# Performance work log

Hardware: AMD Instinct MI355X
Metric: run time of the kernel (lower is better)

Reference implementation:

```python
import jax, jax.numpy as jnp
import numpy as np

D = 1024
H = 16
HD = D // H
INNER = 4 * D
EPS = 1e-5


def layernorm(x, g, b):
    mu = jnp.mean(x, axis=-1, keepdims=True)
    var = jnp.mean(jnp.square(x - mu), axis=-1, keepdims=True)
    return (x - mu) * jax.lax.rsqrt(var + EPS) * g + b


def setup_inputs() -> dict:
    key = jax.random.key(0)
    ks = jax.random.split(key, 12)
    s = 0.02
    return {
        "x": jax.random.normal(ks[0], (2, 2048, D), dtype=jnp.float32),
        "ln1_g": jnp.ones((D,), jnp.float32),
        "ln1_b": jnp.zeros((D,), jnp.float32),
        "Wq": jax.random.normal(ks[1], (D, D), jnp.float32) * s,
        "Wk": jax.random.normal(ks[2], (D, D), jnp.float32) * s,
        "Wv": jax.random.normal(ks[3], (D, D), jnp.float32) * s,
        "Wo": jax.random.normal(ks[4], (D, D), jnp.float32) * s,
        "ln2_g": jnp.ones((D,), jnp.float32),
        "ln2_b": jnp.zeros((D,), jnp.float32),
        "W_up": jax.random.normal(ks[5], (D, INNER), jnp.float32) * s,
        "b_up": jnp.zeros((INNER,), jnp.float32),
        "W_down": jax.random.normal(ks[6], (INNER, D), jnp.float32) * s,
        "b_down": jnp.zeros((D,), jnp.float32),
    }


def reference(x, ln1_g, ln1_b, Wq, Wk, Wv, Wo, ln2_g, ln2_b, W_up, b_up, W_down, b_down):
    B, T, C = x.shape
    # --- attention sub-block (pre-norm) ---
    h = layernorm(x, ln1_g, ln1_b)
    q = (h @ Wq).reshape(B, T, H, HD).transpose(0, 2, 1, 3)  # [B,H,T,HD]
    k = (h @ Wk).reshape(B, T, H, HD).transpose(0, 2, 1, 3)
    v = (h @ Wv).reshape(B, T, H, HD).transpose(0, 2, 1, 3)
    scores = jnp.einsum("bhqd,bhkd->bhqk", q, k) / jnp.sqrt(jnp.float32(HD))
    causal = jnp.tril(jnp.ones((T, T), dtype=bool))
    scores = jnp.where(causal, scores, jnp.finfo(scores.dtype).min)
    weights = jax.nn.softmax(scores, axis=-1)
    ctx = jnp.einsum("bhqk,bhkd->bhqd", weights, v)
    y = ctx.transpose(0, 2, 1, 3).reshape(B, T, C) @ Wo
    x = x + y
    # --- MLP sub-block (pre-norm) ---
    h2 = layernorm(x, ln2_g, ln2_b)
    m = jax.nn.gelu(h2 @ W_up + b_up, approximate=False)  # nn.GELU() default = exact erf
    x = x + (m @ W_down + b_down)
    return x
```

## Files before the change

### kernel.cpp

```cpp
#include <hip/hip_runtime.h>
#include <hip/hip_bf16.h>
#include <math.h>

constexpr int Dm = 1024;
constexpr int Tt = 2048;
constexpr int NB = 2;
constexpr int NHd = 16;
constexpr int HDd = 64;
constexpr int FF = 4096;
constexpr int NTOK = NB * Tt;

typedef __attribute__((ext_vector_type(8))) short bf16x8;
typedef __attribute__((ext_vector_type(4))) float f32x4;

struct alignas(8) bh4 { __hip_bfloat16 x, y, z, w; };

#define GLOAD16(gp, lp)                                                        \
  __builtin_amdgcn_global_load_lds(                                            \
      (const __attribute__((address_space(1))) void*)(gp),                     \
      (__attribute__((address_space(3))) void*)(lp), 16, 0, 0)

__device__ __forceinline__ float wave_sum(float v) {
#pragma unroll
  for (int off = 32; off > 0; off >>= 1) v += __shfl_xor(v, off, 64);
  return v;
}

__device__ __forceinline__ float gelu_f(float x) {
  return 0.5f * x * (1.0f + erff(x * 0.7071067811865475f));
}

__global__ __launch_bounds__(256) void ln_kernel(
    const float* __restrict__ x, const float* __restrict__ g,
    const float* __restrict__ b, __hip_bfloat16* __restrict__ out) {
  __shared__ float red[8];
  const int row = blockIdx.x;
  const int t = threadIdx.x;
  const float4 v = reinterpret_cast<const float4*>(x + (size_t)row * Dm)[t];
  float s = v.x + v.y + v.z + v.w;
  s = wave_sum(s);
  if ((t & 63) == 0) red[t >> 6] = s;
  __syncthreads();
  const float mu = (red[0] + red[1] + red[2] + red[3]) * (1.0f / Dm);
  const float dx = v.x - mu, dy = v.y - mu, dz = v.z - mu, dw = v.w - mu;
  float sq = dx * dx + dy * dy + dz * dz + dw * dw;
  sq = wave_sum(sq);
  if ((t & 63) == 0) red[4 + (t >> 6)] = sq;
  __syncthreads();
  const float var = (red[4] + red[5] + red[6] + red[7]) * (1.0f / Dm);
  const float rstd = 1.0f / sqrtf(var + 1e-5f);
  const float4 gv = reinterpret_cast<const float4*>(g)[t];
  const float4 bv = reinterpret_cast<const float4*>(b)[t];
  bh4 o;
  o.x = __float2bfloat16(dx * rstd * gv.x + bv.x);
  o.y = __float2bfloat16(dy * rstd * gv.y + bv.y);
  o.z = __float2bfloat16(dz * rstd * gv.z + bv.z);
  o.w = __float2bfloat16(dw * rstd * gv.w + bv.w);
  *(bh4*)&out[(size_t)row * Dm + t * 4] = o;
}

__global__ __launch_bounds__(256) void wt_kernel(
    const float* __restrict__ W, __hip_bfloat16* __restrict__ Wt,
    int K, int N) {
  __shared__ float tile[32][33];
  const int n0 = blockIdx.x * 32, k0 = blockIdx.y * 32;
  const int tx = threadIdx.x & 31, ty = threadIdx.x >> 5;
#pragma unroll
  for (int r = 0; r < 4; ++r)
    tile[ty + 8 * r][tx] = W[(size_t)(k0 + ty + 8 * r) * N + n0 + tx];
  __syncthreads();
#pragma unroll
  for (int r = 0; r < 4; ++r)
    Wt[(size_t)(n0 + ty + 8 * r) * K + k0 + tx] =
        __float2bfloat16(tile[tx][ty + 8 * r]);
}

enum { EP_QKV = 0, EP_RESID = 1, EP_GELU = 2, EP_DOWN = 3 };

template <int EP>
__global__ __launch_bounds__(256) void gemm_bf16(
    const __hip_bfloat16* __restrict__ A, const __hip_bfloat16* __restrict__ Bt,
    void* __restrict__ Cout, int N, int K,
    const float* __restrict__ bias, const float* __restrict__ resid) {
  __shared__ alignas(16) __hip_bfloat16 As[128 * 64];
  __shared__ alignas(16) __hip_bfloat16 Bs[128 * 64];
  const int t = threadIdx.x;
  const int wave = t >> 6, lane = t & 63;
  const int m0 = blockIdx.x * 128, n0 = blockIdx.y * 128;
  const int wm = wave >> 1, wn = wave & 1;
  const int srow = wave * 32 + (lane >> 3);
  const int scol = (lane & 7) * 8;
  const __hip_bfloat16* Ag = A + (size_t)(m0 + srow) * K + scol;
  const __hip_bfloat16* Bg = Bt + (size_t)(n0 + srow) * K + scol;
  const int lr = lane & 15, lk = lane >> 4;
  f32x4 acc[4][4] = {};
  for (int k0 = 0; k0 < K; k0 += 64) {
#pragma unroll
    for (int i = 0; i < 4; ++i) {
      GLOAD16(Ag + (size_t)i * 8 * K + k0, &As[wave * 2048 + i * 512]);
      GLOAD16(Bg + (size_t)i * 8 * K + k0, &Bs[wave * 2048 + i * 512]);
    }
    __syncthreads();
#pragma unroll
    for (int ks = 0; ks < 2; ++ks) {
      bf16x8 af[4], bf[4];
#pragma unroll
      for (int mi = 0; mi < 4; ++mi)
        af[mi] = *(const bf16x8*)&As[(wm * 64 + mi * 16 + lr) * 64 + ks * 32 + lk * 8];
#pragma unroll
      for (int ni = 0; ni < 4; ++ni)
        bf[ni] = *(const bf16x8*)&Bs[(wn * 64 + ni * 16 + lr) * 64 + ks * 32 + lk * 8];
#pragma unroll
      for (int mi = 0; mi < 4; ++mi)
#pragma unroll
        for (int ni = 0; ni < 4; ++ni)
          acc[mi][ni] = __builtin_amdgcn_mfma_f32_16x16x32_bf16(
              af[mi], bf[ni], acc[mi][ni], 0, 0, 0);
    }
    __syncthreads();
  }
#pragma unroll
  for (int mi = 0; mi < 4; ++mi) {
#pragma unroll
    for (int ni = 0; ni < 4; ++ni) {
      const int col = n0 + wn * 64 + ni * 16 + lr;
      const int row0 = m0 + wm * 64 + mi * 16 + lk * 4;
#pragma unroll
      for (int j = 0; j < 4; ++j) {
        const int row = row0 + j;
        const float v = acc[mi][ni][j];
        if (EP == EP_QKV) {
          const int which = col >> 10, cc = col & 1023;
          const int head = cc >> 6, hd = cc & 63;
          const int bb = row >> 11, tt2 = row & 2047;
          ((__hip_bfloat16*)Cout)[(size_t)which * (4u << 20) +
              ((size_t)(bb * NHd + head) * Tt + tt2) * HDd + hd] =
              __float2bfloat16(v);
        } else if (EP == EP_RESID) {
          ((float*)Cout)[(size_t)row * N + col] =
              v + resid[(size_t)row * N + col];
        } else if (EP == EP_GELU) {
          ((__hip_bfloat16*)Cout)[(size_t)row * N + col] =
              __float2bfloat16(gelu_f(v + bias[col]));
        } else {
          ((float*)Cout)[(size_t)row * N + col] =
              v + bias[col] + resid[(size_t)row * N + col];
        }
      }
    }
  }
}

__global__ __launch_bounds__(256) void attn_mfma(
    const __hip_bfloat16* __restrict__ Q, const __hip_bfloat16* __restrict__ K,
    const __hip_bfloat16* __restrict__ V, __hip_bfloat16* __restrict__ ctx) {
  __shared__ alignas(16) __hip_bfloat16 Ks[64 * 64];
  __shared__ alignas(16) __hip_bfloat16 VTs[64 * 72];
  __shared__ alignas(16) __hip_bfloat16 Pl[4 * 16 * 72];
  const int qt = (int)gridDim.x - 1 - (int)blockIdx.x;
  const int bh = blockIdx.y;
  const int t = threadIdx.x;
  const int w = t >> 6, l = t & 63;
  const int r = l & 15, g = l >> 4;
  const size_t base = (size_t)bh * (size_t)Tt * HDd;
  bf16x8 qf[2];
  {
    const __hip_bfloat16* qrow = Q + base + (size_t)(qt * 64 + w * 16 + r) * HDd;
    qf[0] = *(const bf16x8*)(qrow + g * 8);
    qf[1] = *(const bf16x8*)(qrow + 32 + g * 8);
  }
  float mrun[4], lrun[4];
  f32x4 oacc[4];
#pragma unroll
  for (int j = 0; j < 4; ++j) { mrun[j] = -1e30f; lrun[j] = 0.0f; }
#pragma unroll
  for (int db = 0; db < 4; ++db) oacc[db] = f32x4{0.f, 0.f, 0.f, 0.f};

  for (int kt = 0; kt <= qt; ++kt) {
    __syncthreads();
    {
      const int kr = t >> 3;
      const int cb = (t & 7) ^ (kr & 7);
#pragma unroll
      for (int i = 0; i < 2; ++i)
        GLOAD16(K + base + (size_t)(kt * 64 + i * 32 + kr) * HDd + cb * 8,
                (char*)Ks + i * 4096 + t * 16);
    }
    {
      const int kv = t >> 2, d0 = (t & 3) * 16;
      const __hip_bfloat16* vr = V + base + (size_t)(kt * 64 + kv) * HDd + d0;
      const bf16x8 v0 = *(const bf16x8*)vr;
      const bf16x8 v1 = *(const bf16x8*)(vr + 8);
      short* vts = (short*)VTs;
#pragma unroll
      for (int j = 0; j < 8; ++j) {
        vts[(d0 + j) * 72 + (kv ^ (j << 3))] = v0[j];
        vts[(d0 + 8 + j) * 72 + (kv ^ (j << 3))] = v1[j];
      }
    }
    __syncthreads();
    f32x4 sacc[4];
#pragma unroll
    for (int c4 = 0; c4 < 4; ++c4) sacc[c4] = f32x4{0.f, 0.f, 0.f, 0.f};
#pragma unroll
    for (int c4 = 0; c4 < 4; ++c4) {
      const int krow = c4 * 16 + r;
#pragma unroll
      for (int ks = 0; ks < 2; ++ks) {
        const int cb = (ks * 4 + g) ^ (krow & 7);
        const bf16x8 kf = *(const bf16x8*)&Ks[krow * 64 + cb * 8];
        sacc[c4] = __builtin_amdgcn_mfma_f32_16x16x32_bf16(
            qf[ks], kf, sacc[c4], 0, 0, 0);
      }
    }
    float sc[4][4];
#pragma unroll
    for (int c4 = 0; c4 < 4; ++c4)
#pragma unroll
      for (int j = 0; j < 4; ++j) {
        float s = sacc[c4][j] * 0.125f;
        if (kt == qt && (c4 * 16 + r) > (w * 16 + g * 4 + j)) s = -1e30f;
        sc[c4][j] = s;
      }
#pragma unroll
    for (int j = 0; j < 4; ++j) {
      float mj = fmaxf(fmaxf(sc[0][j], sc[1][j]), fmaxf(sc[2][j], sc[3][j]));
      mj = fmaxf(mj, __shfl_xor(mj, 1, 64));
      mj = fmaxf(mj, __shfl_xor(mj, 2, 64));
      mj = fmaxf(mj, __shfl_xor(mj, 4, 64));
      mj = fmaxf(mj, __shfl_xor(mj, 8, 64));
      const float mn = fmaxf(mrun[j], mj);
      const float corr = __expf(mrun[j] - mn);
      float rs = 0.0f;
#pragma unroll
      for (int c4 = 0; c4 < 4; ++c4) {
        const float p = __expf(sc[c4][j] - mn);
        rs += p;
        Pl[w * 1152 + (g * 4 + j) * 72 + c4 * 16 + r] = __float2bfloat16(p);
      }
      rs += __shfl_xor(rs, 1, 64);
      rs += __shfl_xor(rs, 2, 64);
      rs += __shfl_xor(rs, 4, 64);
      rs += __shfl_xor(rs, 8, 64);
      lrun[j] = lrun[j] * corr + rs;
      mrun[j] = mn;
#pragma unroll
      for (int db = 0; db < 4; ++db) oacc[db][j] *= corr;
    }
#pragma unroll
    for (int kh = 0; kh < 2; ++kh) {
      const bf16x8 pa = *(const bf16x8*)&Pl[w * 1152 + r * 72 + kh * 32 + g * 8];
#pragma unroll
      for (int db = 0; db < 4; ++db) {
        const int d = db * 16 + r;
        const int cb = (kh * 4 + g) ^ (d & 7);
        const bf16x8 vf = *(const bf16x8*)&VTs[d * 72 + cb * 8];
        oacc[db] = __builtin_amdgcn_mfma_f32_16x16x32_bf16(
            pa, vf, oacc[db], 0, 0, 0);
      }
    }
  }
  const int b = bh >> 4, hh = bh & 15;
#pragma unroll
  for (int j = 0; j < 4; ++j) {
    const float inv = 1.0f / lrun[j];
    const size_t tok = (size_t)b * Tt + qt * 64 + w * 16 + g * 4 + j;
#pragma unroll
    for (int db = 0; db < 4; ++db)
      ctx[tok * Dm + hh * 64 + db * 16 + r] =
          __float2bfloat16(oacc[db][j] * inv);
  }
}

extern "C" void kernel_launch(void* const* d_in, const int* in_sizes, int n_in,
                              void* d_out, int out_size, void* d_ws, size_t ws_size,
                              hipStream_t stream) {
  (void)in_sizes; (void)n_in; (void)out_size; (void)ws_size;
  const float* x   = (const float*)d_in[0];
  const float* g1  = (const float*)d_in[1];
  const float* b1  = (const float*)d_in[2];
  const float* Wq  = (const float*)d_in[3];
  const float* Wk  = (const float*)d_in[4];
  const float* Wv  = (const float*)d_in[5];
  const float* Wo  = (const float*)d_in[6];
  const float* g2  = (const float*)d_in[7];
  const float* b2  = (const float*)d_in[8];
  const float* Wup = (const float*)d_in[9];
  const float* bup = (const float*)d_in[10];
  const float* Wdn = (const float*)d_in[11];
  const float* bdn = (const float*)d_in[12];
  float* out = (float*)d_out;
  char* ws = (char*)d_ws;

  __hip_bfloat16* h    = (__hip_bfloat16*)(ws);
  __hip_bfloat16* qkv  = (__hip_bfloat16*)(ws + (8ull << 20));
  __hip_bfloat16* ctx  = (__hip_bfloat16*)(ws + (32ull << 20));
  float*          x1   = (float*)(ws + (40ull << 20));
  __hip_bfloat16* mbuf = (__hip_bfloat16*)(ws + (8ull << 20));
  __hip_bfloat16* WtQ  = (__hip_bfloat16*)(ws + (56ull << 20));
  __hip_bfloat16* WtO  = (__hip_bfloat16*)(ws + (62ull << 20));
  __hip_bfloat16* WtUp = (__hip_bfloat16*)(ws + (64ull << 20));
  __hip_bfloat16* WtDn = (__hip_bfloat16*)(ws + (72ull << 20));

  wt_kernel<<<dim3(32, 32), 256, 0, stream>>>(Wq, WtQ, 1024, 1024);
  wt_kernel<<<dim3(32, 32), 256, 0, stream>>>(Wk, WtQ + (1u << 20), 1024, 1024);
  wt_kernel<<<dim3(32, 32), 256, 0, stream>>>(Wv, WtQ + (2u << 20), 1024, 1024);
  wt_kernel<<<dim3(32, 32), 256, 0, stream>>>(Wo, WtO, 1024, 1024);
  wt_kernel<<<dim3(128, 32), 256, 0, stream>>>(Wup, WtUp, 1024, 4096);
  wt_kernel<<<dim3(32, 128), 256, 0, stream>>>(Wdn, WtDn, 4096, 1024);

  ln_kernel<<<NTOK, 256, 0, stream>>>(x, g1, b1, h);
  gemm_bf16<EP_QKV><<<dim3(32, 24), 256, 0, stream>>>(
      h, WtQ, qkv, 3072, 1024, nullptr, nullptr);
  attn_mfma<<<dim3(32, 32), 256, 0, stream>>>(
      qkv, qkv + (4u << 20), qkv + (8u << 20), ctx);
  gemm_bf16<EP_RESID><<<dim3(32, 8), 256, 0, stream>>>(
      ctx, WtO, x1, 1024, 1024, nullptr, x);
  ln_kernel<<<NTOK, 256, 0, stream>>>(x1, g2, b2, h);
  gemm_bf16<EP_GELU><<<dim3(32, 32), 256, 0, stream>>>(
      h, WtUp, mbuf, 4096, 1024, bup, nullptr);
  gemm_bf16<EP_DOWN><<<dim3(32, 8), 256, 0, stream>>>(
      mbuf, WtDn, out, 1024, 4096, bdn, x1);
}
```

Baseline: 514.3 us.

## Pair causal query tiles per block and transpose score layout in attention

Each attention block now handles two query tiles (qp and 31-qp), which balances the triangular causal work across blocks and halves the grid. The QK MFMA operands are swapped so each lane owns one query row. Row max and sum then need only two cross-lane shuffles instead of four per row. V is transposed into LDS as packed bf16 pairs with a new swizzle, and the P buffer is XOR-swizzled to reduce bank conflicts. The risks are lower occupancy from having only 512 blocks, and added correctness risk in the new mask and swizzle indexing.

```diff
diff --git a/kernel.cpp b/kernel.cpp
--- a/kernel.cpp
+++ b/kernel.cpp
@@ -155,120 +155,129 @@
     const __hip_bfloat16* __restrict__ Q, const __hip_bfloat16* __restrict__ K,
     const __hip_bfloat16* __restrict__ V, __hip_bfloat16* __restrict__ ctx) {
   __shared__ alignas(16) __hip_bfloat16 Ks[64 * 64];
-  __shared__ alignas(16) __hip_bfloat16 VTs[64 * 72];
-  __shared__ alignas(16) __hip_bfloat16 Pl[4 * 16 * 72];
-  const int qt = (int)gridDim.x - 1 - (int)blockIdx.x;
+  __shared__ alignas(16) unsigned int VTu[64 * 36];
+  __shared__ alignas(16) __hip_bfloat16 Pl[4][16 * 72];
+  const int qp = blockIdx.x;
   const int bh = blockIdx.y;
   const int t = threadIdx.x;
   const int w = t >> 6, l = t & 63;
   const int r = l & 15, g = l >> 4;
+  const int rho = r & 7;
   const size_t base = (size_t)bh * (size_t)Tt * HDd;
-  bf16x8 qf[2];
-  {
-    const __hip_bfloat16* qrow = Q + base + (size_t)(qt * 64 + w * 16 + r) * HDd;
-    qf[0] = *(const bf16x8*)(qrow + g * 8);
-    qf[1] = *(const bf16x8*)(qrow + 32 + g * 8);
-  }
-  float mrun[4], lrun[4];
-  f32x4 oacc[4];
-#pragma unroll
-  for (int j = 0; j < 4; ++j) { mrun[j] = -1e30f; lrun[j] = 0.0f; }
-#pragma unroll
-  for (int db = 0; db < 4; ++db) oacc[db] = f32x4{0.f, 0.f, 0.f, 0.f};
-
-  for (int kt = 0; kt <= qt; ++kt) {
-    __syncthreads();
+
+#pragma unroll 1
+  for (int ph = 0; ph < 2; ++ph) {
+    const int qt = ph ? (31 - qp) : qp;
+    bf16x8 qf[2];
     {
-      const int kr = t >> 3;
-      const int cb = (t & 7) ^ (kr & 7);
-#pragma unroll
-      for (int i = 0; i < 2; ++i)
-        GLOAD16(K + base + (size_t)(kt * 64 + i * 32 + kr) * HDd + cb * 8,
-                (char*)Ks + i * 4096 + t * 16);
-    }
-    {
-      const int kv = t >> 2, d0 = (t & 3) * 16;
-      const __hip_bfloat16* vr = V + base + (size_t)(kt * 64 + kv) * HDd + d0;
-      const bf16x8 v0 = *(const bf16x8*)vr;
-      const bf16x8 v1 = *(const bf16x8*)(vr + 8);
-      short* vts = (short*)VTs;
-#pragma unroll
-      for (int j = 0; j < 8; ++j) {
-        vts[(d0 + j) * 72 + (kv ^ (j << 3))] = v0[j];
-        vts[(d0 + 8 + j) * 72 + (kv ^ (j << 3))] = v1[j];
-      }
-    }
-    __syncthreads();
-    f32x4 sacc[4];
-#pragma unroll
-    for (int c4 = 0; c4 < 4; ++c4) sacc[c4] = f32x4{0.f, 0.f, 0.f, 0.f};
-#pragma unroll
-    for (int c4 = 0; c4 < 4; ++c4) {
-      const int krow = c4 * 16 + r;
-#pragma unroll
-      for (int ks = 0; ks < 2; ++ks) {
-        const int cb = (ks * 4 + g) ^ (krow & 7);
-        const bf16x8 kf = *(const bf16x8*)&Ks[krow * 64 + cb * 8];
-        sacc[c4] = __builtin_amdgcn_mfma_f32_16x16x32_bf16(
-            qf[ks], kf, sacc[c4], 0, 0, 0);
-      }
-    }
-    float sc[4][4];
-#pragma unroll
-    for (int c4 = 0; c4 < 4; ++c4)
+      const __hip_bfloat16* qrow = Q + base + (size_t)(qt * 64 + w * 16 + r) * HDd;
+      qf[0] = *(const bf16x8*)(qrow + g * 8);
+      qf[1] = *(const bf16x8*)(qrow + 32 + g * 8);
+    }
+    float mrun = -1e30f, lrun = 0.0f;
+    f32x4 oacc[4];
+#pragma unroll
+    for (int db = 0; db < 4; ++db) oacc[db] = f32x4{0.f, 0.f, 0.f, 0.f};
+
+    for (int kt = 0; kt <= qt; ++kt) {
+      __syncthreads();
+      {
+        const int kr = t >> 3;
+        const int cb = (t & 7) ^ (kr & 7);
+#pragma unroll
+        for (int i = 0; i < 2; ++i)
+          GLOAD16(K + base + (size_t)(kt * 64 + i * 32 + kr) * HDd + cb * 8,
+                  (char*)Ks + i * 4096 + t * 16);
+      }
+      {
+        const int kvp = t >> 3, dblk = t & 7;
+        const __hip_bfloat16* vr =
+            V + base + (size_t)(kt * 64 + kvp * 2) * HDd + dblk * 8;
+        const bf16x8 v0 = *(const bf16x8*)vr;
+        const bf16x8 v1 = *(const bf16x8*)(vr + HDd);
+        const int kvs = kvp ^ (dblk << 2);
+#pragma unroll
+        for (int j = 0; j < 8; ++j) {
+          const unsigned int pk = (unsigned int)(unsigned short)v0[j] |
+                                  ((unsigned int)(unsigned short)v1[j] << 16);
+          VTu[(dblk * 8 + j) * 36 + kvs] = pk;
+        }
+      }
+      __syncthreads();
+      f32x4 sacc[4];
+#pragma unroll
+      for (int c4 = 0; c4 < 4; ++c4) sacc[c4] = f32x4{0.f, 0.f, 0.f, 0.f};
+#pragma unroll
+      for (int c4 = 0; c4 < 4; ++c4) {
+        const int krow = c4 * 16 + r;
+#pragma unroll
+        for (int ks = 0; ks < 2; ++ks) {
+          const int cb = (ks * 4 + g) ^ (krow & 7);
+          const bf16x8 kf = *(const bf16x8*)&Ks[krow * 64 + cb * 8];
+          sacc[c4] = __builtin_amdgcn_mfma_f32_16x16x32_bf16(
+              kf, qf[ks], sacc[c4], 0, 0, 0);
+        }
+      }
+      float sc[16];
+      float pm = -1e30f;
+#pragma unroll
+      for (int c4 = 0; c4 < 4; ++c4)
+#pragma unroll
+        for (int j = 0; j < 4; ++j) {
+          float s = sacc[c4][j] * 0.125f;
+          if (kt == qt && (c4 * 16 + g * 4 + j) > (w * 16 + r)) s = -1e30f;
+          sc[c4 * 4 + j] = s;
+          pm = fmaxf(pm, s);
+        }
+      pm = fmaxf(pm, __shfl_xor(pm, 16, 64));
+      pm = fmaxf(pm, __shfl_xor(pm, 32, 64));
+      const float mn = fmaxf(mrun, pm);
+      const float corr = __expf(mrun - mn);
+      mrun = mn;
+      float ps = 0.0f;
+#pragma unroll
+      for (int c4 = 0; c4 < 4; ++c4)
+#pragma unroll
+        for (int j = 0; j < 4; ++j) {
+          const float p = __expf(sc[c4 * 4 + j] - mn);
+          ps += p;
+          Pl[w][r * 72 + ((c4 * 16 + g * 4 + j) ^ (rho << 3))] =
+              __float2bfloat16(p);
+        }
+      ps += __shfl_xor(ps, 16, 64);
+      ps += __shfl_xor(ps, 32, 64);
+      lrun = lrun * corr + ps;
 #pragma unroll
       for (int j = 0; j < 4; ++j) {
-        float s = sacc[c4][j] * 0.125f;
-        if (kt == qt && (c4 * 16 + r) > (w * 16 + g * 4 + j)) s = -1e30f;
-        sc[c4][j] = s;
-      }
+        const float cj = __shfl(corr, g * 4 + j, 64);
+#pragma unroll
+        for (int db = 0; db < 4; ++db) oacc[db][j] *= cj;
+      }
+#pragma unroll
+      for (int kh = 0; kh < 2; ++kh) {
+        const bf16x8 pa =
+            *(const bf16x8*)&Pl[w][r * 72 + ((kh * 32 + g * 8) ^ (rho << 3))];
+#pragma unroll
+        for (int db = 0; db < 4; ++db) {
+          const int d = db * 16 + r;
+          const bf16x8 vf = *(const bf16x8*)&VTu[d * 36 +
+              (((kh * 4 + g) << 2) ^ ((d >> 3) << 2))];
+          oacc[db] = __builtin_amdgcn_mfma_f32_16x16x32_bf16(
+              pa, vf, oacc[db], 0, 0, 0);
+        }
+      }
+    }
+    const int b = bh >> 4, hh = bh & 15;
 #pragma unroll
     for (int j = 0; j < 4; ++j) {
-      float mj = fmaxf(fmaxf(sc[0][j], sc[1][j]), fmaxf(sc[2][j], sc[3][j]));
-      mj = fmaxf(mj, __shfl_xor(mj, 1, 64));
-      mj = fmaxf(mj, __shfl_xor(mj, 2, 64));
-      mj = fmaxf(mj, __shfl_xor(mj, 4, 64));
-      mj = fmaxf(mj, __shfl_xor(mj, 8, 64));
-      const float mn = fmaxf(mrun[j], mj);
-      const float corr = __expf(mrun[j] - mn);
-      float rs = 0.0f;
-#pragma unroll
-      for (int c4 = 0; c4 < 4; ++c4) {
-        const float p = __expf(sc[c4][j] - mn);
-        rs += p;
-        Pl[w * 1152 + (g * 4 + j) * 72 + c4 * 16 + r] = __float2bfloat16(p);
-      }
-      rs += __shfl_xor(rs, 1, 64);
-      rs += __shfl_xor(rs, 2, 64);
-      rs += __shfl_xor(rs, 4, 64);
-      rs += __shfl_xor(rs, 8, 64);
-      lrun[j] = lrun[j] * corr + rs;
-      mrun[j] = mn;
-#pragma unroll
-      for (int db = 0; db < 4; ++db) oacc[db][j] *= corr;
-    }
-#pragma unroll
-    for (int kh = 0; kh < 2; ++kh) {
-      const bf16x8 pa = *(const bf16x8*)&Pl[w * 1152 + r * 72 + kh * 32 + g * 8];
-#pragma unroll
-      for (int db = 0; db < 4; ++db) {
-        const int d = db * 16 + r;
-        const int cb = (kh * 4 + g) ^ (d & 7);
-        const bf16x8 vf = *(const bf16x8*)&VTs[d * 72 + cb * 8];
-        oacc[db] = __builtin_amdgcn_mfma_f32_16x16x32_bf16(
-            pa, vf, oacc[db], 0, 0, 0);
-      }
-    }
-  }
-  const int b = bh >> 4, hh = bh & 15;
-#pragma unroll
-  for (int j = 0; j < 4; ++j) {
-    const float inv = 1.0f / lrun[j];
-    const size_t tok = (size_t)b * Tt + qt * 64 + w * 16 + g * 4 + j;
-#pragma unroll
-    for (int db = 0; db < 4; ++db)
-      ctx[tok * Dm + hh * 64 + db * 16 + r] =
-          __float2bfloat16(oacc[db][j] * inv);
+      const float lj = __shfl(lrun, g * 4 + j, 64);
+      const float inv = 1.0f / lj;
+      const size_t tok = (size_t)b * Tt + qt * 64 + w * 16 + g * 4 + j;
+#pragma unroll
+      for (int db = 0; db < 4; ++db)
+        ctx[tok * Dm + hh * 64 + db * 16 + r] =
+            __float2bfloat16(oacc[db][j] * inv);
+    }
   }
 }
 
@@ -312,7 +321,7 @@
   ln_kernel<<<NTOK, 256, 0, stream>>>(x, g1, b1, h);
   gemm_bf16<EP_QKV><<<dim3(32, 24), 256, 0, stream>>>(
       h, WtQ, qkv, 3072, 1024, nullptr, nullptr);
-  attn_mfma<<<dim3(32, 32), 256, 0, stream>>>(
+  attn_mfma<<<dim3(16, 32), 256, 0, stream>>>(
       qkv, qkv + (4u << 20), qkv + (8u << 20), ctx);
   gemm_bf16<EP_RESID><<<dim3(32, 8), 256, 0, stream>>>(
       ctx, WtO, x1, 1024, 1024, nullptr, x);
```

New measurement: 441.8 us. 14.1% less time.
